# Performance work log

Hardware: AMD Instinct MI355X
Metric: run time of the kernel (lower is better)

The kernel has to match this reference:

```python
import jax, jax.numpy as jnp
import numpy as np

HIDDEN = 2048
N_EXPERTS = 8
TOP_K = 2
MOE_INTER = 1408
NORM_TOPK = False  # config.norm_topk_prob


def setup_inputs() -> dict:
    key = jax.random.key(0)
    k0, k1, k2, k3, k4 = jax.random.split(key, 5)
    hidden_states = jax.random.normal(k0, (2, 2048, HIDDEN), dtype=jnp.float32)
    # router gate: nn.Linear(hidden, num_experts, bias=False) -> store as [H, E]
    gate_w = jax.random.normal(k1, (HIDDEN, N_EXPERTS), dtype=jnp.float32) * 0.02
    # per-expert MLP weights, stacked over experts (Linear is x @ W.T, stored pre-transposed)
    w_gate = jax.random.normal(k2, (N_EXPERTS, HIDDEN, MOE_INTER), dtype=jnp.float32) * 0.02
    w_up = jax.random.normal(k3, (N_EXPERTS, HIDDEN, MOE_INTER), dtype=jnp.float32) * 0.02
    w_down = jax.random.normal(k4, (N_EXPERTS, MOE_INTER, HIDDEN), dtype=jnp.float32) * 0.02
    return {"hidden_states": hidden_states, "gate_w": gate_w,
            "w_gate": w_gate, "w_up": w_up, "w_down": w_down}


def reference(hidden_states, gate_w, w_gate, w_up, w_down):
    B, S, H = hidden_states.shape
    x = hidden_states.reshape(-1, H)                      # [T, H]
    T = x.shape[0]
    router_logits = x @ gate_w                            # [T, E]
    probs = jax.nn.softmax(router_logits.astype(jnp.float32), axis=-1)
    routing_weights, selected = jax.lax.top_k(probs, TOP_K)  # [T, K], [T, K]
    if NORM_TOPK:
        routing_weights = routing_weights / routing_weights.sum(-1, keepdims=True)
    routing_weights = routing_weights.astype(x.dtype)
    # dense combine weights [T, E]: scatter top-k weights to expert slots
    combine = jnp.zeros((T, N_EXPERTS), dtype=x.dtype)
    combine = combine.at[jnp.arange(T)[:, None], selected].add(routing_weights)
    # run all experts densely (reference form of gather-MLP-scatter)
    g = jnp.einsum('th,ehf->tef', x, w_gate)              # [T, E, F]
    u = jnp.einsum('th,ehf->tef', x, w_up)
    h = jax.nn.silu(g) * u
    y = jnp.einsum('tef,efh->teh', h, w_down)             # [T, E, H]
    out = jnp.einsum('te,teh->th', combine, y)            # [T, H]
    return out
```

## Files before the change

### kernel.cpp

```cpp
#include <hip/hip_runtime.h>
#include <hip/hip_bf16.h>

#define HID  2048
#define NEXP 8
#define FINT 1408
#define TM   256
#define BK   32
#define GU_NPAN 88
#define DN_NPAN 64

typedef __bf16 bf16_t;
typedef __bf16 bf16x8 __attribute__((ext_vector_type(8)));
typedef float  f32x4  __attribute__((ext_vector_type(4)));

#define AS1 __attribute__((address_space(1)))
#define AS3 __attribute__((address_space(3)))

__device__ __forceinline__ void gll16(const void* g, void* l) {
    __builtin_amdgcn_global_load_lds((const AS1 void*)g, (AS3 void*)l, 16, 0, 0);
}

#define VMCNT4() asm volatile("s_waitcnt vmcnt(4)" ::: "memory")
#define VMCNT0() asm volatile("s_waitcnt vmcnt(0)" ::: "memory")
#define SB0() __builtin_amdgcn_sched_barrier(0)

__global__ __launch_bounds__(64) void router_kernel(
    const float* __restrict__ x, const float* __restrict__ gw,
    int* __restrict__ cnt, int* __restrict__ topk_id, float* __restrict__ topk_w,
    bf16_t* __restrict__ xb, int T)
{
    int t = blockIdx.x;
    if (t >= T) return;
    int lane = threadIdx.x;
    float acc[NEXP];
#pragma unroll
    for (int e = 0; e < NEXP; ++e) acc[e] = 0.f;
    const float* xr = x + (size_t)t * HID;
    bf16_t* xo = xb + (size_t)t * HID;
    for (int i = lane; i < HID; i += 64) {
        float xv = xr[i];
        xo[i] = (bf16_t)xv;
        const float4* g4 = (const float4*)(gw + (size_t)i * NEXP);
        float4 a = g4[0], b = g4[1];
        acc[0] += xv * a.x; acc[1] += xv * a.y; acc[2] += xv * a.z; acc[3] += xv * a.w;
        acc[4] += xv * b.x; acc[5] += xv * b.y; acc[6] += xv * b.z; acc[7] += xv * b.w;
    }
#pragma unroll
    for (int d = 1; d < 64; d <<= 1) {
#pragma unroll
        for (int e = 0; e < NEXP; ++e) acc[e] += __shfl_xor(acc[e], d, 64);
    }
    float mx = acc[0];
#pragma unroll
    for (int e = 1; e < NEXP; ++e) mx = fmaxf(mx, acc[e]);
    float p[NEXP]; float s = 0.f;
#pragma unroll
    for (int e = 0; e < NEXP; ++e) { p[e] = expf(acc[e] - mx); s += p[e]; }
    float inv = 1.f / s;
    int i1 = 0;
#pragma unroll
    for (int e = 1; e < NEXP; ++e) if (acc[e] > acc[i1]) i1 = e;
    int i2 = (i1 == 0) ? 1 : 0;
#pragma unroll
    for (int e = 0; e < NEXP; ++e) if (e != i1 && acc[e] > acc[i2]) i2 = e;
    if (lane == 0) {
        topk_id[t * 2 + 0] = i1; topk_id[t * 2 + 1] = i2;
        topk_w[t * 2 + 0] = p[i1] * inv; topk_w[t * 2 + 1] = p[i2] * inv;
        atomicAdd(&cnt[i1], 1); atomicAdd(&cnt[i2], 1);
    }
}

__global__ void offsets_kernel(const int* __restrict__ cnt, int* __restrict__ offs,
                               int* __restrict__ gbase, int* __restrict__ gcount,
                               int* __restrict__ dbase, int* __restrict__ dcount,
                               int* __restrict__ gu, int* __restrict__ dn)
{
    if (threadIdx.x == 0) {
        int s = 0;
        for (int e = 0; e < NEXP; ++e) { offs[e] = s; s += cnt[e]; }
        offs[NEXP] = s;
        int k = 0;
        for (int x = 0; x < 8; ++x) {
            gbase[x] = k;
            for (int p = x; p < GU_NPAN; p += 8) {
                int e = p / 11, fp = p - e * 11;
                int nt = (cnt[e] + TM - 1) / TM;
                for (int t = 0; t < nt; ++t) gu[k++] = (e << 10) | (fp << 6) | t;
            }
            gcount[x] = k - gbase[x];
        }
        k = 0;
        for (int x = 0; x < 8; ++x) {
            dbase[x] = k;
            for (int p = x; p < DN_NPAN; p += 8) {
                int e = p >> 3, hp = p & 7;
                int nt = (cnt[e] + TM - 1) / TM;
                for (int t = 0; t < nt; ++t) dn[k++] = (e << 10) | (hp << 6) | t;
            }
            dcount[x] = k - dbase[x];
        }
    }
}

__global__ void scatter_kernel(
    const int* __restrict__ topk_id, const int* __restrict__ offs, int* __restrict__ fill,
    int* __restrict__ tok, int* __restrict__ slot_of, int T)
{
    int t = blockIdx.x * blockDim.x + threadIdx.x;
    if (t >= T) return;
#pragma unroll
    for (int k = 0; k < 2; ++k) {
        int e = topk_id[t * 2 + k];
        int pos = atomicAdd(&fill[e], 1);
        int slot = offs[e] + pos;
        tok[slot] = t;
        slot_of[t * 2 + k] = slot;
    }
}

__global__ __launch_bounds__(256) void cvt_t_kernel(
    const float* __restrict__ in, bf16_t* __restrict__ outb, int R, int C)
{
    int tilesR = R >> 6, tilesC = C >> 6;
    int per = tilesR * tilesC;
    int e = blockIdx.x / per;
    int rem = blockIdx.x - e * per;
    int tr = rem / tilesC, tc = rem - tr * tilesC;
    const float* src = in + (size_t)e * R * C + (size_t)(tr * 64) * C + tc * 64;
    bf16_t* dst = outb + (size_t)e * R * C + (size_t)(tc * 64) * R + tr * 64;

    __shared__ float tile[64][65];
    int tid = threadIdx.x;
    int rr = tid >> 4;
    int cc = (tid & 15) * 4;
#pragma unroll
    for (int i = 0; i < 4; ++i) {
        float4 v = *(const float4*)(src + (size_t)(rr + i * 16) * C + cc);
        tile[rr + i * 16][cc + 0] = v.x; tile[rr + i * 16][cc + 1] = v.y;
        tile[rr + i * 16][cc + 2] = v.z; tile[rr + i * 16][cc + 3] = v.w;
    }
    __syncthreads();
    int oc = tid >> 2;
    int og = (tid & 3) * 16;
    bf16_t* dp = dst + (size_t)oc * R + og;
    bf16x8 o0, o1;
#pragma unroll
    for (int j = 0; j < 8; ++j) { o0[j] = (bf16_t)tile[og + j][oc]; o1[j] = (bf16_t)tile[og + 8 + j][oc]; }
    *(bf16x8*)dp = o0;
    *(bf16x8*)(dp + 8) = o1;
}

__global__ __launch_bounds__(512, 2) void gateup3_kernel(
    const bf16_t* __restrict__ xb, const bf16_t* __restrict__ wgb, const bf16_t* __restrict__ wub,
    const int* __restrict__ offs, const int* __restrict__ tok,
    const int* __restrict__ gbase, const int* __restrict__ gcount, const int* __restrict__ gu,
    bf16_t* __restrict__ h_buf)
{
    __shared__ bf16_t smem[49152];
    const int tid = threadIdx.x;
    const int lane = tid & 63, w = tid >> 6;
    const int wm = w >> 1, wn = w & 1;
    const int lr = lane & 15, lg = lane >> 4;
    const int rl = lane >> 2;
    const int sw8 = ((lane & 3) ^ ((lane >> 3) & 3)) * 8;
    const int ksw = (lg ^ ((lr >> 1) & 3)) * 8;

    const int xcd = blockIdx.x & 7, slot = blockIdx.x >> 3;
    const int icnt = gcount[xcd], ib = gbase[xcd];

    for (int ii = slot; ii < icnt; ii += 32) {
        const int it = gu[ib + ii];
        const int e = it >> 10, fp = (it >> 6) & 15, tr = it & 63;
        const int seg0 = offs[e];
        const int rbase = tr * TM;
        const int nvalid = min(offs[e + 1] - seg0 - rbase, TM);
        const int row0 = seg0 + rbase;
        const int f0 = fp * 128;

        const bf16_t* aP[2];
#pragma unroll
        for (int i = 0; i < 2; ++i) {
            int r = (w * 2 + i) * 16 + rl;
            int tk = tok[row0 + min(r, nvalid - 1)];
            aP[i] = xb + (size_t)tk * HID + sw8;
        }
        const bf16_t* bP[2];
#pragma unroll
        for (int i = 0; i < 2; ++i) {
            int br = (w * 2 + i) * 16 + rl;
            const bf16_t* W = (br < 128) ? wgb : wub;
            bP[i] = W + ((size_t)e * FINT + f0 + (br & 127)) * HID + sw8;
        }

        f32x4 acc[4][8];
#pragma unroll
        for (int mi = 0; mi < 4; ++mi)
#pragma unroll
            for (int ni = 0; ni < 8; ++ni) acc[mi][ni] = (f32x4){0.f, 0.f, 0.f, 0.f};

        auto STAGE = [&](int b, int kt) {
            int k0 = kt * BK;
            bf16_t* A = smem + b * 8192;
            bf16_t* B = smem + 24576 + b * 8192;
            gll16(aP[0] + k0, A + (w * 2 + 0) * 512);
            gll16(aP[1] + k0, A + (w * 2 + 1) * 512);
            gll16(bP[0] + k0, B + (w * 2 + 0) * 512);
            gll16(bP[1] + k0, B + (w * 2 + 1) * 512);
        };
        auto COMPUTE = [&](int b) {
            const bf16_t* A = smem + b * 8192;
            const bf16_t* B = smem + 24576 + b * 8192;
            bf16x8 bfr[8];
#pragma unroll
            for (int ni = 0; ni < 8; ++ni)
                bfr[ni] = *(const bf16x8*)&B[(wn * 128 + ni * 16 + lr) * BK + ksw];
#pragma unroll
            for (int mi = 0; mi < 4; ++mi) {
                bf16x8 a = *(const bf16x8*)&A[(wm * 64 + mi * 16 + lr) * BK + ksw];
#pragma unroll
                for (int ni = 0; ni < 8; ++ni)
                    acc[mi][ni] = __builtin_amdgcn_mfma_f32_16x16x32_bf16(a, bfr[ni], acc[mi][ni], 0, 0, 0);
            }
        };

        const int NK = HID / BK;
        STAGE(0, 0); STAGE(1, 1);
        int c0 = 0, c1 = 1, c2 = 2;
        for (int kt = 0; kt < NK; ++kt) {
            SB0();
            if (kt + 1 < NK) { VMCNT4(); } else { VMCNT0(); }
            __builtin_amdgcn_s_barrier();
            SB0();
            if (kt + 2 < NK) STAGE(c2, kt + 2);
            SB0();
            COMPUTE(c0);
            int t = c0; c0 = c1; c1 = c2; c2 = t;
        }
        __syncthreads();

        if (wn == 1) {
#pragma unroll
            for (int mi = 0; mi < 4; ++mi)
#pragma unroll
                for (int ni = 0; ni < 8; ++ni)
#pragma unroll
                    for (int rr = 0; rr < 4; ++rr) {
                        int row = wm * 64 + mi * 16 + lg * 4 + rr;
                        int col = ni * 16 + lr;
                        smem[row * 128 + col] = (bf16_t)acc[mi][ni][rr];
                    }
        }
        __syncthreads();
        if (wn == 0) {
#pragma unroll
            for (int mi = 0; mi < 4; ++mi)
#pragma unroll
                for (int ni = 0; ni < 8; ++ni)
#pragma unroll
                    for (int rr = 0; rr < 4; ++rr) {
                        int row = wm * 64 + mi * 16 + lg * 4 + rr;
                        int col = ni * 16 + lr;
                        float g = acc[mi][ni][rr];
                        float u = (float)smem[row * 128 + col];
                        float h = (g / (1.f + __expf(-g))) * u;
                        if (row < nvalid)
                            h_buf[(size_t)(row0 + row) * FINT + f0 + col] = (bf16_t)h;
                    }
        }
        __syncthreads();
    }
}

__global__ __launch_bounds__(512, 2) void down3_kernel(
    const bf16_t* __restrict__ h_buf, const bf16_t* __restrict__ wdb,
    const int* __restrict__ offs,
    const int* __restrict__ dbase, const int* __restrict__ dcount, const int* __restrict__ dn,
    bf16_t* __restrict__ y_buf)
{
    __shared__ bf16_t smem[49152];
    const int tid = threadIdx.x;
    const int lane = tid & 63, w = tid >> 6;
    const int wm = w >> 1, wn = w & 1;
    const int lr = lane & 15, lg = lane >> 4;
    const int rl = lane >> 2;
    const int sw8 = ((lane & 3) ^ ((lane >> 3) & 3)) * 8;
    const int ksw = (lg ^ ((lr >> 1) & 3)) * 8;

    const int xcd = blockIdx.x & 7, slot = blockIdx.x >> 3;
    const int icnt = dcount[xcd], ib = dbase[xcd];

    for (int ii = slot; ii < icnt; ii += 32) {
        const int it = dn[ib + ii];
        const int e = it >> 10, hp = (it >> 6) & 15, tr = it & 63;
        const int seg0 = offs[e];
        const int rbase = tr * TM;
        const int nvalid = min(offs[e + 1] - seg0 - rbase, TM);
        const int row0 = seg0 + rbase;
        const int h0 = hp * 256;

        const bf16_t* aP[2];
#pragma unroll
        for (int i = 0; i < 2; ++i) {
            int r = (w * 2 + i) * 16 + rl;
            aP[i] = h_buf + (size_t)(row0 + r) * FINT + sw8;
        }
        const bf16_t* bP[2];
#pragma unroll
        for (int i = 0; i < 2; ++i) {
            int br = (w * 2 + i) * 16 + rl;
            bP[i] = wdb + ((size_t)e * HID + h0 + br) * FINT + sw8;
        }

        f32x4 acc[4][8];
#pragma unroll
        for (int mi = 0; mi < 4; ++mi)
#pragma unroll
            for (int ni = 0; ni < 8; ++ni) acc[mi][ni] = (f32x4){0.f, 0.f, 0.f, 0.f};

        auto STAGE = [&](int b, int kt) {
            int k0 = kt * BK;
            bf16_t* A = smem + b * 8192;
            bf16_t* B = smem + 24576 + b * 8192;
            gll16(aP[0] + k0, A + (w * 2 + 0) * 512);
            gll16(aP[1] + k0, A + (w * 2 + 1) * 512);
            gll16(bP[0] + k0, B + (w * 2 + 0) * 512);
            gll16(bP[1] + k0, B + (w * 2 + 1) * 512);
        };
        auto COMPUTE = [&](int b) {
            const bf16_t* A = smem + b * 8192;
            const bf16_t* B = smem + 24576 + b * 8192;
            bf16x8 bfr[8];
#pragma unroll
            for (int ni = 0; ni < 8; ++ni)
                bfr[ni] = *(const bf16x8*)&B[(wn * 128 + ni * 16 + lr) * BK + ksw];
#pragma unroll
            for (int mi = 0; mi < 4; ++mi) {
                bf16x8 a = *(const bf16x8*)&A[(wm * 64 + mi * 16 + lr) * BK + ksw];
#pragma unroll
                for (int ni = 0; ni < 8; ++ni)
                    acc[mi][ni] = __builtin_amdgcn_mfma_f32_16x16x32_bf16(a, bfr[ni], acc[mi][ni], 0, 0, 0);
            }
        };

        const int NK = FINT / BK;
        STAGE(0, 0); STAGE(1, 1);
        int c0 = 0, c1 = 1, c2 = 2;
        for (int kt = 0; kt < NK; ++kt) {
            SB0();
            if (kt + 1 < NK) { VMCNT4(); } else { VMCNT0(); }
            __builtin_amdgcn_s_barrier();
            SB0();
            if (kt + 2 < NK) STAGE(c2, kt + 2);
            SB0();
            COMPUTE(c0);
            int t = c0; c0 = c1; c1 = c2; c2 = t;
        }

#pragma unroll
        for (int mi = 0; mi < 4; ++mi)
#pragma unroll
            for (int ni = 0; ni < 8; ++ni)
#pragma unroll
                for (int rr = 0; rr < 4; ++rr) {
                    int row = wm * 64 + mi * 16 + lg * 4 + rr;
                    int col = wn * 128 + ni * 16 + lr;
                    if (row < nvalid)
                        y_buf[(size_t)(row0 + row) * HID + h0 + col] = (bf16_t)acc[mi][ni][rr];
                }
        __syncthreads();
    }
}

__global__ __launch_bounds__(256) void combine_kernel(
    const bf16_t* __restrict__ y, const int* __restrict__ slot_of,
    const float* __restrict__ topk_w, float* __restrict__ out, int T)
{
    int t = blockIdx.x;
    int tid = threadIdx.x;
    int s0 = slot_of[t * 2], s1 = slot_of[t * 2 + 1];
    float w0 = topk_w[t * 2], w1 = topk_w[t * 2 + 1];
    const bf16x8* y0 = (const bf16x8*)(y + (size_t)s0 * HID);
    const bf16x8* y1 = (const bf16x8*)(y + (size_t)s1 * HID);
    bf16x8 v0 = y0[tid], v1 = y1[tid];
    float* op = out + (size_t)t * HID + tid * 8;
#pragma unroll
    for (int j = 0; j < 8; ++j)
        op[j] = w0 * (float)v0[j] + w1 * (float)v1[j];
}

extern "C" void kernel_launch(void* const* d_in, const int* in_sizes, int n_in,
                              void* d_out, int out_size, void* d_ws, size_t ws_size,
                              hipStream_t stream)
{
    const float* x  = (const float*)d_in[0];
    const float* gw = (const float*)d_in[1];
    const float* wg = (const float*)d_in[2];
    const float* wu = (const float*)d_in[3];
    const float* wd = (const float*)d_in[4];
    float* out = (float*)d_out;
    int T = in_sizes[0] / HID;
    int S2 = 2 * T;

    char* base = (char*)d_ws;
    int* cnt     = (int*)base;
    int* fill    = cnt + 8;
    int* offs    = cnt + 16;
    int* gbase   = cnt + 32;
    int* gcount  = cnt + 40;
    int* dbase   = cnt + 48;
    int* dcount  = cnt + 56;
    int* gu      = cnt + 64;
    int* dnl     = cnt + 576;
    int* topk_id = cnt + 960;
    float* topk_w = (float*)(topk_id + S2);
    int* tok     = (int*)(topk_w + S2);
    int* slot_of = tok + S2 + 256;
    size_t small_end = (size_t)((char*)(slot_of + S2) - base);
    size_t cur = (small_end + 255) & ~(size_t)255;
    auto take = [&](size_t bytes) -> size_t {
        size_t o = cur; cur += bytes; cur = (cur + 255) & ~(size_t)255; return o;
    };
    size_t wbytes = (size_t)NEXP * HID * FINT * 2;
    size_t o_xb  = take((size_t)T * HID * 2);
    size_t o_wgb = take(wbytes);
    size_t o_wub = take(wbytes);
    size_t o_wdb = take(wbytes);
    size_t o_h   = take((size_t)(S2 + 256) * FINT * 2);
    size_t o_y   = take((size_t)(S2 + 256) * HID * 2);
    (void)ws_size;

    bf16_t* xb    = (bf16_t*)(base + o_xb);
    bf16_t* wgb   = (bf16_t*)(base + o_wgb);
    bf16_t* wub   = (bf16_t*)(base + o_wub);
    bf16_t* wdb   = (bf16_t*)(base + o_wdb);
    bf16_t* h_buf = (bf16_t*)(base + o_h);
    bf16_t* y_buf = (bf16_t*)(base + o_y);

    hipMemsetAsync(base, 0, 64, stream);

    router_kernel<<<T, 64, 0, stream>>>(x, gw, cnt, topk_id, topk_w, xb, T);
    offsets_kernel<<<1, 64, 0, stream>>>(cnt, offs, gbase, gcount, dbase, dcount, gu, dnl);
    scatter_kernel<<<(T + 255) / 256, 256, 0, stream>>>(topk_id, offs, fill, tok, slot_of, T);

    int gridW = NEXP * (HID / 64) * (FINT / 64);
    cvt_t_kernel<<<gridW, 256, 0, stream>>>(wg, wgb, HID, FINT);
    cvt_t_kernel<<<gridW, 256, 0, stream>>>(wu, wub, HID, FINT);
    cvt_t_kernel<<<gridW, 256, 0, stream>>>(wd, wdb, FINT, HID);

    gateup3_kernel<<<256, 512, 0, stream>>>(xb, wgb, wub, offs, tok, gbase, gcount, gu, h_buf);
    down3_kernel<<<256, 512, 0, stream>>>(h_buf, wdb, offs, dbase, dcount, dnl, y_buf);
    combine_kernel<<<T, 256, 0, stream>>>(y_buf, slot_of, topk_w, out, T);
}
```

Before: 493.4 us.

## Interleave split B staging with MFMA halves, fuse weight converts, parallelize offsets

The GEMM main loops in both expert kernels now split the B-tile global-to-LDS staging into two halves. Each half is interleaved with one half of the MFMA work, using explicit lgkmcnt waits and s_setprio to raise wave priority during the MFMA blocks. This also cuts live B fragment registers from 8 to 4. The three weight convert-transpose launches are merged into one kernel, and the offsets kernel builds its schedule lists with 16 threads instead of one, reducing launch and serial overhead. The lgkmcnt(0) waits could serialize LDS reads with the MFMAs.

```diff
diff --git a/kernel.cpp b/kernel.cpp
--- a/kernel.cpp
+++ b/kernel.cpp
@@ -22,6 +22,7 @@
 
 #define VMCNT4() asm volatile("s_waitcnt vmcnt(4)" ::: "memory")
 #define VMCNT0() asm volatile("s_waitcnt vmcnt(0)" ::: "memory")
+#define LGKM0()  asm volatile("s_waitcnt lgkmcnt(0)" ::: "memory")
 #define SB0() __builtin_amdgcn_sched_barrier(0)
 
 __global__ __launch_bounds__(64) void router_kernel(
@@ -75,29 +76,43 @@
                                int* __restrict__ dbase, int* __restrict__ dcount,
                                int* __restrict__ gu, int* __restrict__ dn)
 {
-    if (threadIdx.x == 0) {
+    __shared__ int gc[8], dc[8];
+    int tid = threadIdx.x;
+    if (tid == 0) {
         int s = 0;
         for (int e = 0; e < NEXP; ++e) { offs[e] = s; s += cnt[e]; }
         offs[NEXP] = s;
-        int k = 0;
-        for (int x = 0; x < 8; ++x) {
-            gbase[x] = k;
-            for (int p = x; p < GU_NPAN; p += 8) {
-                int e = p / 11, fp = p - e * 11;
-                int nt = (cnt[e] + TM - 1) / TM;
-                for (int t = 0; t < nt; ++t) gu[k++] = (e << 10) | (fp << 6) | t;
-            }
-            gcount[x] = k - gbase[x];
-        }
-        k = 0;
-        for (int x = 0; x < 8; ++x) {
-            dbase[x] = k;
-            for (int p = x; p < DN_NPAN; p += 8) {
-                int e = p >> 3, hp = p & 7;
-                int nt = (cnt[e] + TM - 1) / TM;
-                for (int t = 0; t < nt; ++t) dn[k++] = (e << 10) | (hp << 6) | t;
-            }
-            dcount[x] = k - dbase[x];
+    }
+    if (tid < 8) {
+        int c = 0;
+        for (int p = tid; p < GU_NPAN; p += 8) { int e = p / 11; c += (cnt[e] + TM - 1) / TM; }
+        gc[tid] = c;
+    } else if (tid < 16) {
+        int x = tid - 8, c = 0;
+        for (int p = x; p < DN_NPAN; p += 8) { int e = p >> 3; c += (cnt[e] + TM - 1) / TM; }
+        dc[x] = c;
+    }
+    __syncthreads();
+    if (tid < 8) {
+        int base = 0;
+        for (int i = 0; i < tid; ++i) base += gc[i];
+        gbase[tid] = base; gcount[tid] = gc[tid];
+        int k = base;
+        for (int p = tid; p < GU_NPAN; p += 8) {
+            int e = p / 11, fp = p - e * 11;
+            int nt = (cnt[e] + TM - 1) / TM;
+            for (int t = 0; t < nt; ++t) gu[k++] = (e << 10) | (fp << 6) | t;
+        }
+    } else if (tid < 16) {
+        int x = tid - 8;
+        int base = 0;
+        for (int i = 0; i < x; ++i) base += dc[i];
+        dbase[x] = base; dcount[x] = dc[x];
+        int k = base;
+        for (int p = x; p < DN_NPAN; p += 8) {
+            int e = p >> 3, hp = p & 7;
+            int nt = (cnt[e] + TM - 1) / TM;
+            for (int t = 0; t < nt; ++t) dn[k++] = (e << 10) | (hp << 6) | t;
         }
     }
 }
@@ -118,13 +133,21 @@
     }
 }
 
-__global__ __launch_bounds__(256) void cvt_t_kernel(
-    const float* __restrict__ in, bf16_t* __restrict__ outb, int R, int C)
-{
-    int tilesR = R >> 6, tilesC = C >> 6;
-    int per = tilesR * tilesC;
-    int e = blockIdx.x / per;
-    int rem = blockIdx.x - e * per;
+__global__ __launch_bounds__(256) void cvt3_kernel(
+    const float* __restrict__ wg, const float* __restrict__ wu, const float* __restrict__ wd,
+    bf16_t* __restrict__ wgb, bf16_t* __restrict__ wub, bf16_t* __restrict__ wdb)
+{
+    const int per = NEXP * (HID / 64) * (FINT / 64);
+    int b = blockIdx.x;
+    const float* in; bf16_t* outb; int R, C;
+    if (b < per)            { in = wg; outb = wgb; R = HID;  C = FINT; }
+    else if (b < 2 * per)   { b -= per; in = wu; outb = wub; R = HID;  C = FINT; }
+    else                    { b -= 2 * per; in = wd; outb = wdb; R = FINT; C = HID; }
+
+    int tilesC = C >> 6;
+    int perE = (R >> 6) * tilesC;
+    int e = b / perE;
+    int rem = b - e * perE;
     int tr = rem / tilesC, tc = rem - tr * tilesC;
     const float* src = in + (size_t)e * R * C + (size_t)(tr * 64) * C + tc * 64;
     bf16_t* dst = outb + (size_t)e * R * C + (size_t)(tc * 64) * R + tr * 64;
@@ -198,42 +221,59 @@
 #pragma unroll
             for (int ni = 0; ni < 8; ++ni) acc[mi][ni] = (f32x4){0.f, 0.f, 0.f, 0.f};
 
-        auto STAGE = [&](int b, int kt) {
+        auto STAGE_A = [&](int b, int kt) {
             int k0 = kt * BK;
             bf16_t* A = smem + b * 8192;
-            bf16_t* B = smem + 24576 + b * 8192;
             gll16(aP[0] + k0, A + (w * 2 + 0) * 512);
             gll16(aP[1] + k0, A + (w * 2 + 1) * 512);
+        };
+        auto STAGE_B = [&](int b, int kt) {
+            int k0 = kt * BK;
+            bf16_t* B = smem + 24576 + b * 8192;
             gll16(bP[0] + k0, B + (w * 2 + 0) * 512);
             gll16(bP[1] + k0, B + (w * 2 + 1) * 512);
         };
-        auto COMPUTE = [&](int b) {
-            const bf16_t* A = smem + b * 8192;
-            const bf16_t* B = smem + 24576 + b * 8192;
-            bf16x8 bfr[8];
-#pragma unroll
-            for (int ni = 0; ni < 8; ++ni)
-                bfr[ni] = *(const bf16x8*)&B[(wn * 128 + ni * 16 + lr) * BK + ksw];
-#pragma unroll
-            for (int mi = 0; mi < 4; ++mi) {
-                bf16x8 a = *(const bf16x8*)&A[(wm * 64 + mi * 16 + lr) * BK + ksw];
-#pragma unroll
-                for (int ni = 0; ni < 8; ++ni)
-                    acc[mi][ni] = __builtin_amdgcn_mfma_f32_16x16x32_bf16(a, bfr[ni], acc[mi][ni], 0, 0, 0);
-            }
-        };
 
         const int NK = HID / BK;
-        STAGE(0, 0); STAGE(1, 1);
+        STAGE_A(0, 0); STAGE_B(0, 0); STAGE_A(1, 1); STAGE_B(1, 1);
         int c0 = 0, c1 = 1, c2 = 2;
         for (int kt = 0; kt < NK; ++kt) {
             SB0();
             if (kt + 1 < NK) { VMCNT4(); } else { VMCNT0(); }
             __builtin_amdgcn_s_barrier();
             SB0();
-            if (kt + 2 < NK) STAGE(c2, kt + 2);
-            SB0();
-            COMPUTE(c0);
+            const bf16_t* A = smem + c0 * 8192;
+            const bf16_t* B = smem + 24576 + c0 * 8192;
+            if (kt + 2 < NK) STAGE_A(c2, kt + 2);
+            bf16x8 afr[4], bfr[4];
+#pragma unroll
+            for (int mi = 0; mi < 4; ++mi)
+                afr[mi] = *(const bf16x8*)&A[(wm * 64 + mi * 16 + lr) * BK + ksw];
+#pragma unroll
+            for (int ni = 0; ni < 4; ++ni)
+                bfr[ni] = *(const bf16x8*)&B[(wn * 128 + ni * 16 + lr) * BK + ksw];
+            LGKM0(); SB0();
+            __builtin_amdgcn_s_setprio(1);
+#pragma unroll
+            for (int mi = 0; mi < 4; ++mi)
+#pragma unroll
+                for (int ni = 0; ni < 4; ++ni)
+                    acc[mi][ni] = __builtin_amdgcn_mfma_f32_16x16x32_bf16(afr[mi], bfr[ni], acc[mi][ni], 0, 0, 0);
+            __builtin_amdgcn_s_setprio(0);
+            SB0();
+            if (kt + 2 < NK) STAGE_B(c2, kt + 2);
+#pragma unroll
+            for (int ni = 0; ni < 4; ++ni)
+                bfr[ni] = *(const bf16x8*)&B[(wn * 128 + (ni + 4) * 16 + lr) * BK + ksw];
+            LGKM0(); SB0();
+            __builtin_amdgcn_s_setprio(1);
+#pragma unroll
+            for (int mi = 0; mi < 4; ++mi)
+#pragma unroll
+                for (int ni = 0; ni < 4; ++ni)
+                    acc[mi][ni + 4] = __builtin_amdgcn_mfma_f32_16x16x32_bf16(afr[mi], bfr[ni], acc[mi][ni + 4], 0, 0, 0);
+            __builtin_amdgcn_s_setprio(0);
+            SB0();
             int t = c0; c0 = c1; c1 = c2; c2 = t;
         }
         __syncthreads();
@@ -317,42 +357,59 @@
 #pragma unroll
             for (int ni = 0; ni < 8; ++ni) acc[mi][ni] = (f32x4){0.f, 0.f, 0.f, 0.f};
 
-        auto STAGE = [&](int b, int kt) {
+        auto STAGE_A = [&](int b, int kt) {
             int k0 = kt * BK;
             bf16_t* A = smem + b * 8192;
-            bf16_t* B = smem + 24576 + b * 8192;
             gll16(aP[0] + k0, A + (w * 2 + 0) * 512);
             gll16(aP[1] + k0, A + (w * 2 + 1) * 512);
+        };
+        auto STAGE_B = [&](int b, int kt) {
+            int k0 = kt * BK;
+            bf16_t* B = smem + 24576 + b * 8192;
             gll16(bP[0] + k0, B + (w * 2 + 0) * 512);
             gll16(bP[1] + k0, B + (w * 2 + 1) * 512);
         };
-        auto COMPUTE = [&](int b) {
-            const bf16_t* A = smem + b * 8192;
-            const bf16_t* B = smem + 24576 + b * 8192;
-            bf16x8 bfr[8];
-#pragma unroll
-            for (int ni = 0; ni < 8; ++ni)
-                bfr[ni] = *(const bf16x8*)&B[(wn * 128 + ni * 16 + lr) * BK + ksw];
-#pragma unroll
-            for (int mi = 0; mi < 4; ++mi) {
-                bf16x8 a = *(const bf16x8*)&A[(wm * 64 + mi * 16 + lr) * BK + ksw];
-#pragma unroll
-                for (int ni = 0; ni < 8; ++ni)
-                    acc[mi][ni] = __builtin_amdgcn_mfma_f32_16x16x32_bf16(a, bfr[ni], acc[mi][ni], 0, 0, 0);
-            }
-        };
 
         const int NK = FINT / BK;
-        STAGE(0, 0); STAGE(1, 1);
+        STAGE_A(0, 0); STAGE_B(0, 0); STAGE_A(1, 1); STAGE_B(1, 1);
         int c0 = 0, c1 = 1, c2 = 2;
         for (int kt = 0; kt < NK; ++kt) {
             SB0();
             if (kt + 1 < NK) { VMCNT4(); } else { VMCNT0(); }
             __builtin_amdgcn_s_barrier();
             SB0();
-            if (kt + 2 < NK) STAGE(c2, kt + 2);
-            SB0();
-            COMPUTE(c0);
+            const bf16_t* A = smem + c0 * 8192;
+            const bf16_t* B = smem + 24576 + c0 * 8192;
+            if (kt + 2 < NK) STAGE_A(c2, kt + 2);
+            bf16x8 afr[4], bfr[4];
+#pragma unroll
+            for (int mi = 0; mi < 4; ++mi)
+                afr[mi] = *(const bf16x8*)&A[(wm * 64 + mi * 16 + lr) * BK + ksw];
+#pragma unroll
+            for (int ni = 0; ni < 4; ++ni)
+                bfr[ni] = *(const bf16x8*)&B[(wn * 128 + ni * 16 + lr) * BK + ksw];
+            LGKM0(); SB0();
+            __builtin_amdgcn_s_setprio(1);
+#pragma unroll
+            for (int mi = 0; mi < 4; ++mi)
+#pragma unroll
+                for (int ni = 0; ni < 4; ++ni)
+                    acc[mi][ni] = __builtin_amdgcn_mfma_f32_16x16x32_bf16(afr[mi], bfr[ni], acc[mi][ni], 0, 0, 0);
+            __builtin_amdgcn_s_setprio(0);
+            SB0();
+            if (kt + 2 < NK) STAGE_B(c2, kt + 2);
+#pragma unroll
+            for (int ni = 0; ni < 4; ++ni)
+                bfr[ni] = *(const bf16x8*)&B[(wn * 128 + (ni + 4) * 16 + lr) * BK + ksw];
+            LGKM0(); SB0();
+            __builtin_amdgcn_s_setprio(1);
+#pragma unroll
+            for (int mi = 0; mi < 4; ++mi)
+#pragma unroll
+                for (int ni = 0; ni < 4; ++ni)
+                    acc[mi][ni + 4] = __builtin_amdgcn_mfma_f32_16x16x32_bf16(afr[mi], bfr[ni], acc[mi][ni + 4], 0, 0, 0);
+            __builtin_amdgcn_s_setprio(0);
+            SB0();
             int t = c0; c0 = c1; c1 = c2; c2 = t;
         }
 
@@ -442,10 +499,8 @@
     offsets_kernel<<<1, 64, 0, stream>>>(cnt, offs, gbase, gcount, dbase, dcount, gu, dnl);
     scatter_kernel<<<(T + 255) / 256, 256, 0, stream>>>(topk_id, offs, fill, tok, slot_of, T);
 
-    int gridW = NEXP * (HID / 64) * (FINT / 64);
-    cvt_t_kernel<<<gridW, 256, 0, stream>>>(wg, wgb, HID, FINT);
-    cvt_t_kernel<<<gridW, 256, 0, stream>>>(wu, wub, HID, FINT);
-    cvt_t_kernel<<<gridW, 256, 0, stream>>>(wd, wdb, FINT, HID);
+    int gridW = 3 * NEXP * (HID / 64) * (FINT / 64);
+    cvt3_kernel<<<gridW, 256, 0, stream>>>(wg, wu, wd, wgb, wub, wdb);
 
     gateup3_kernel<<<256, 512, 0, stream>>>(xb, wgb, wub, offs, tok, gbase, gcount, gu, h_buf);
     down3_kernel<<<256, 512, 0, stream>>>(h_buf, wdb, offs, dbase, dcount, dnl, y_buf);
```

Result: faster. 469.4 us (-4.9%).

## Fuse router and weight conversion, double-buffer GEMMs for higher occupancy

Applied to the files above, without the earlier changes.

The router and the three weight transpose/convert launches are merged into one prep kernel, and the router now handles four tokens per block with vectorized loads. Both grouped GEMMs drop from triple to double buffering, which cuts LDS use so four blocks fit per CU, and they launch with twice the grid. The offsets kernel is parallelized across 16 threads. The cost is an extra barrier per k-step and a shallower prefetch pipeline, which may expose more load latency.

```diff
diff --git a/kernel.cpp b/kernel.cpp
--- a/kernel.cpp
+++ b/kernel.cpp
@@ -23,51 +23,100 @@
 #define VMCNT4() asm volatile("s_waitcnt vmcnt(4)" ::: "memory")
 #define VMCNT0() asm volatile("s_waitcnt vmcnt(0)" ::: "memory")
 #define SB0() __builtin_amdgcn_sched_barrier(0)
-
-__global__ __launch_bounds__(64) void router_kernel(
+#define BAR() __builtin_amdgcn_s_barrier()
+
+__global__ __launch_bounds__(256) void prep_kernel(
     const float* __restrict__ x, const float* __restrict__ gw,
     int* __restrict__ cnt, int* __restrict__ topk_id, float* __restrict__ topk_w,
-    bf16_t* __restrict__ xb, int T)
-{
-    int t = blockIdx.x;
-    if (t >= T) return;
-    int lane = threadIdx.x;
-    float acc[NEXP];
-#pragma unroll
-    for (int e = 0; e < NEXP; ++e) acc[e] = 0.f;
-    const float* xr = x + (size_t)t * HID;
-    bf16_t* xo = xb + (size_t)t * HID;
-    for (int i = lane; i < HID; i += 64) {
-        float xv = xr[i];
-        xo[i] = (bf16_t)xv;
-        const float4* g4 = (const float4*)(gw + (size_t)i * NEXP);
-        float4 a = g4[0], b = g4[1];
-        acc[0] += xv * a.x; acc[1] += xv * a.y; acc[2] += xv * a.z; acc[3] += xv * a.w;
-        acc[4] += xv * b.x; acc[5] += xv * b.y; acc[6] += xv * b.z; acc[7] += xv * b.w;
-    }
-#pragma unroll
-    for (int d = 1; d < 64; d <<= 1) {
-#pragma unroll
-        for (int e = 0; e < NEXP; ++e) acc[e] += __shfl_xor(acc[e], d, 64);
-    }
-    float mx = acc[0];
-#pragma unroll
-    for (int e = 1; e < NEXP; ++e) mx = fmaxf(mx, acc[e]);
-    float p[NEXP]; float s = 0.f;
-#pragma unroll
-    for (int e = 0; e < NEXP; ++e) { p[e] = expf(acc[e] - mx); s += p[e]; }
-    float inv = 1.f / s;
-    int i1 = 0;
-#pragma unroll
-    for (int e = 1; e < NEXP; ++e) if (acc[e] > acc[i1]) i1 = e;
-    int i2 = (i1 == 0) ? 1 : 0;
-#pragma unroll
-    for (int e = 0; e < NEXP; ++e) if (e != i1 && acc[e] > acc[i2]) i2 = e;
-    if (lane == 0) {
-        topk_id[t * 2 + 0] = i1; topk_id[t * 2 + 1] = i2;
-        topk_w[t * 2 + 0] = p[i1] * inv; topk_w[t * 2 + 1] = p[i2] * inv;
-        atomicAdd(&cnt[i1], 1); atomicAdd(&cnt[i2], 1);
-    }
+    bf16_t* __restrict__ xb, int T,
+    const float* __restrict__ wg, const float* __restrict__ wu, const float* __restrict__ wd,
+    bf16_t* __restrict__ wgb, bf16_t* __restrict__ wub, bf16_t* __restrict__ wdb)
+{
+    const int RB = T / 4;
+    const int per = NEXP * (HID / 64) * (FINT / 64);
+    __shared__ float tile[64][65];
+
+    if ((int)blockIdx.x < RB) {
+        int tid = threadIdx.x;
+        int lane = tid & 63, w = tid >> 6;
+        int t = blockIdx.x * 4 + w;
+        if (t >= T) return;
+        float acc[NEXP];
+#pragma unroll
+        for (int e = 0; e < NEXP; ++e) acc[e] = 0.f;
+        const float* xr = x + (size_t)t * HID;
+        bf16_t* xo = xb + (size_t)t * HID;
+        for (int i0 = lane * 4; i0 < HID; i0 += 256) {
+            float4 xv = *(const float4*)(xr + i0);
+            bf16_t b4[4] = {(bf16_t)xv.x, (bf16_t)xv.y, (bf16_t)xv.z, (bf16_t)xv.w};
+            *(uint2*)(xo + i0) = *(uint2*)b4;
+            float xs[4] = {xv.x, xv.y, xv.z, xv.w};
+#pragma unroll
+            for (int u = 0; u < 4; ++u) {
+                const float4* g4 = (const float4*)(gw + (size_t)(i0 + u) * NEXP);
+                float4 a = g4[0], b = g4[1];
+                acc[0] += xs[u] * a.x; acc[1] += xs[u] * a.y; acc[2] += xs[u] * a.z; acc[3] += xs[u] * a.w;
+                acc[4] += xs[u] * b.x; acc[5] += xs[u] * b.y; acc[6] += xs[u] * b.z; acc[7] += xs[u] * b.w;
+            }
+        }
+#pragma unroll
+        for (int d = 1; d < 64; d <<= 1) {
+#pragma unroll
+            for (int e = 0; e < NEXP; ++e) acc[e] += __shfl_xor(acc[e], d, 64);
+        }
+        float mx = acc[0];
+#pragma unroll
+        for (int e = 1; e < NEXP; ++e) mx = fmaxf(mx, acc[e]);
+        float p[NEXP]; float s = 0.f;
+#pragma unroll
+        for (int e = 0; e < NEXP; ++e) { p[e] = expf(acc[e] - mx); s += p[e]; }
+        float inv = 1.f / s;
+        int i1 = 0;
+#pragma unroll
+        for (int e = 1; e < NEXP; ++e) if (acc[e] > acc[i1]) i1 = e;
+        int i2 = (i1 == 0) ? 1 : 0;
+#pragma unroll
+        for (int e = 0; e < NEXP; ++e) if (e != i1 && acc[e] > acc[i2]) i2 = e;
+        if (lane == 0) {
+            topk_id[t * 2 + 0] = i1; topk_id[t * 2 + 1] = i2;
+            topk_w[t * 2 + 0] = p[i1] * inv; topk_w[t * 2 + 1] = p[i2] * inv;
+            atomicAdd(&cnt[i1], 1); atomicAdd(&cnt[i2], 1);
+        }
+        return;
+    }
+
+    int b = blockIdx.x - RB;
+    const float* in; bf16_t* outb; int R, C;
+    if (b < per)            { in = wg; outb = wgb; R = HID;  C = FINT; }
+    else if (b < 2 * per)   { b -= per; in = wu; outb = wub; R = HID;  C = FINT; }
+    else                    { b -= 2 * per; in = wd; outb = wdb; R = FINT; C = HID; }
+
+    int tilesC = C >> 6;
+    int perE = (R >> 6) * tilesC;
+    int e = b / perE;
+    int rem = b - e * perE;
+    int tr = rem / tilesC, tc = rem - tr * tilesC;
+    const float* src = in + (size_t)e * R * C + (size_t)(tr * 64) * C + tc * 64;
+    bf16_t* dst = outb + (size_t)e * R * C + (size_t)(tc * 64) * R + tr * 64;
+
+    int tid = threadIdx.x;
+    int rr = tid >> 4;
+    int cc = (tid & 15) * 4;
+#pragma unroll
+    for (int i = 0; i < 4; ++i) {
+        float4 v = *(const float4*)(src + (size_t)(rr + i * 16) * C + cc);
+        tile[rr + i * 16][cc + 0] = v.x; tile[rr + i * 16][cc + 1] = v.y;
+        tile[rr + i * 16][cc + 2] = v.z; tile[rr + i * 16][cc + 3] = v.w;
+    }
+    __syncthreads();
+    int oc = tid >> 2;
+    int og = (tid & 3) * 16;
+    bf16_t* dp = dst + (size_t)oc * R + og;
+    bf16x8 o0, o1;
+#pragma unroll
+    for (int j = 0; j < 8; ++j) { o0[j] = (bf16_t)tile[og + j][oc]; o1[j] = (bf16_t)tile[og + 8 + j][oc]; }
+    *(bf16x8*)dp = o0;
+    *(bf16x8*)(dp + 8) = o1;
 }
 
 __global__ void offsets_kernel(const int* __restrict__ cnt, int* __restrict__ offs,
@@ -75,29 +124,43 @@
                                int* __restrict__ dbase, int* __restrict__ dcount,
                                int* __restrict__ gu, int* __restrict__ dn)
 {
-    if (threadIdx.x == 0) {
+    __shared__ int gc[8], dc[8];
+    int tid = threadIdx.x;
+    if (tid == 0) {
         int s = 0;
         for (int e = 0; e < NEXP; ++e) { offs[e] = s; s += cnt[e]; }
         offs[NEXP] = s;
-        int k = 0;
-        for (int x = 0; x < 8; ++x) {
-            gbase[x] = k;
-            for (int p = x; p < GU_NPAN; p += 8) {
-                int e = p / 11, fp = p - e * 11;
-                int nt = (cnt[e] + TM - 1) / TM;
-                for (int t = 0; t < nt; ++t) gu[k++] = (e << 10) | (fp << 6) | t;
-            }
-            gcount[x] = k - gbase[x];
-        }
-        k = 0;
-        for (int x = 0; x < 8; ++x) {
-            dbase[x] = k;
-            for (int p = x; p < DN_NPAN; p += 8) {
-                int e = p >> 3, hp = p & 7;
-                int nt = (cnt[e] + TM - 1) / TM;
-                for (int t = 0; t < nt; ++t) dn[k++] = (e << 10) | (hp << 6) | t;
-            }
-            dcount[x] = k - dbase[x];
+    }
+    if (tid < 8) {
+        int c = 0;
+        for (int p = tid; p < GU_NPAN; p += 8) { int e = p / 11; c += (cnt[e] + TM - 1) / TM; }
+        gc[tid] = c;
+    } else if (tid < 16) {
+        int x = tid - 8, c = 0;
+        for (int p = x; p < DN_NPAN; p += 8) { int e = p >> 3; c += (cnt[e] + TM - 1) / TM; }
+        dc[x] = c;
+    }
+    __syncthreads();
+    if (tid < 8) {
+        int base = 0;
+        for (int i = 0; i < tid; ++i) base += gc[i];
+        gbase[tid] = base; gcount[tid] = gc[tid];
+        int k = base;
+        for (int p = tid; p < GU_NPAN; p += 8) {
+            int e = p / 11, fp = p - e * 11;
+            int nt = (cnt[e] + TM - 1) / TM;
+            for (int t = 0; t < nt; ++t) gu[k++] = (e << 10) | (fp << 6) | t;
+        }
+    } else if (tid < 16) {
+        int x = tid - 8;
+        int base = 0;
+        for (int i = 0; i < x; ++i) base += dc[i];
+        dbase[x] = base; dcount[x] = dc[x];
+        int k = base;
+        for (int p = x; p < DN_NPAN; p += 8) {
+            int e = p >> 3, hp = p & 7;
+            int nt = (cnt[e] + TM - 1) / TM;
+            for (int t = 0; t < nt; ++t) dn[k++] = (e << 10) | (hp << 6) | t;
         }
     }
 }
@@ -118,45 +181,13 @@
     }
 }
 
-__global__ __launch_bounds__(256) void cvt_t_kernel(
-    const float* __restrict__ in, bf16_t* __restrict__ outb, int R, int C)
-{
-    int tilesR = R >> 6, tilesC = C >> 6;
-    int per = tilesR * tilesC;
-    int e = blockIdx.x / per;
-    int rem = blockIdx.x - e * per;
-    int tr = rem / tilesC, tc = rem - tr * tilesC;
-    const float* src = in + (size_t)e * R * C + (size_t)(tr * 64) * C + tc * 64;
-    bf16_t* dst = outb + (size_t)e * R * C + (size_t)(tc * 64) * R + tr * 64;
-
-    __shared__ float tile[64][65];
-    int tid = threadIdx.x;
-    int rr = tid >> 4;
-    int cc = (tid & 15) * 4;
-#pragma unroll
-    for (int i = 0; i < 4; ++i) {
-        float4 v = *(const float4*)(src + (size_t)(rr + i * 16) * C + cc);
-        tile[rr + i * 16][cc + 0] = v.x; tile[rr + i * 16][cc + 1] = v.y;
-        tile[rr + i * 16][cc + 2] = v.z; tile[rr + i * 16][cc + 3] = v.w;
-    }
-    __syncthreads();
-    int oc = tid >> 2;
-    int og = (tid & 3) * 16;
-    bf16_t* dp = dst + (size_t)oc * R + og;
-    bf16x8 o0, o1;
-#pragma unroll
-    for (int j = 0; j < 8; ++j) { o0[j] = (bf16_t)tile[og + j][oc]; o1[j] = (bf16_t)tile[og + 8 + j][oc]; }
-    *(bf16x8*)dp = o0;
-    *(bf16x8*)(dp + 8) = o1;
-}
-
-__global__ __launch_bounds__(512, 2) void gateup3_kernel(
+__global__ __launch_bounds__(512, 4) void gateup6_kernel(
     const bf16_t* __restrict__ xb, const bf16_t* __restrict__ wgb, const bf16_t* __restrict__ wub,
     const int* __restrict__ offs, const int* __restrict__ tok,
     const int* __restrict__ gbase, const int* __restrict__ gcount, const int* __restrict__ gu,
     bf16_t* __restrict__ h_buf)
 {
-    __shared__ bf16_t smem[49152];
+    __shared__ bf16_t smem[32768];
     const int tid = threadIdx.x;
     const int lane = tid & 63, w = tid >> 6;
     const int wm = w >> 1, wn = w & 1;
@@ -168,7 +199,7 @@
     const int xcd = blockIdx.x & 7, slot = blockIdx.x >> 3;
     const int icnt = gcount[xcd], ib = gbase[xcd];
 
-    for (int ii = slot; ii < icnt; ii += 32) {
+    for (int ii = slot; ii < icnt; ii += 64) {
         const int it = gu[ib + ii];
         const int e = it >> 10, fp = (it >> 6) & 15, tr = it & 63;
         const int seg0 = offs[e];
@@ -201,7 +232,7 @@
         auto STAGE = [&](int b, int kt) {
             int k0 = kt * BK;
             bf16_t* A = smem + b * 8192;
-            bf16_t* B = smem + 24576 + b * 8192;
+            bf16_t* B = smem + 16384 + b * 8192;
             gll16(aP[0] + k0, A + (w * 2 + 0) * 512);
             gll16(aP[1] + k0, A + (w * 2 + 1) * 512);
             gll16(bP[0] + k0, B + (w * 2 + 0) * 512);
@@ -209,7 +240,7 @@
         };
         auto COMPUTE = [&](int b) {
             const bf16_t* A = smem + b * 8192;
-            const bf16_t* B = smem + 24576 + b * 8192;
+            const bf16_t* B = smem + 16384 + b * 8192;
             bf16x8 bfr[8];
 #pragma unroll
             for (int ni = 0; ni < 8; ++ni)
@@ -224,17 +255,19 @@
         };
 
         const int NK = HID / BK;
-        STAGE(0, 0); STAGE(1, 1);
-        int c0 = 0, c1 = 1, c2 = 2;
+        STAGE(0, 0);
+        int cur = 0;
         for (int kt = 0; kt < NK; ++kt) {
-            SB0();
-            if (kt + 1 < NK) { VMCNT4(); } else { VMCNT0(); }
-            __builtin_amdgcn_s_barrier();
-            SB0();
-            if (kt + 2 < NK) STAGE(c2, kt + 2);
-            SB0();
-            COMPUTE(c0);
-            int t = c0; c0 = c1; c1 = c2; c2 = t;
+            const bool nl = (kt + 1 < NK);
+            if (nl) STAGE(cur ^ 1, kt + 1);
+            SB0();
+            if (nl) { VMCNT4(); } else { VMCNT0(); }
+            BAR();
+            SB0();
+            COMPUTE(cur);
+            SB0();
+            BAR();
+            cur ^= 1;
         }
         __syncthreads();
 
@@ -271,13 +304,13 @@
     }
 }
 
-__global__ __launch_bounds__(512, 2) void down3_kernel(
+__global__ __launch_bounds__(512, 4) void down6_kernel(
     const bf16_t* __restrict__ h_buf, const bf16_t* __restrict__ wdb,
     const int* __restrict__ offs,
     const int* __restrict__ dbase, const int* __restrict__ dcount, const int* __restrict__ dn,
     bf16_t* __restrict__ y_buf)
 {
-    __shared__ bf16_t smem[49152];
+    __shared__ bf16_t smem[32768];
     const int tid = threadIdx.x;
     const int lane = tid & 63, w = tid >> 6;
     const int wm = w >> 1, wn = w & 1;
@@ -289,7 +322,7 @@
     const int xcd = blockIdx.x & 7, slot = blockIdx.x >> 3;
     const int icnt = dcount[xcd], ib = dbase[xcd];
 
-    for (int ii = slot; ii < icnt; ii += 32) {
+    for (int ii = slot; ii < icnt; ii += 64) {
         const int it = dn[ib + ii];
         const int e = it >> 10, hp = (it >> 6) & 15, tr = it & 63;
         const int seg0 = offs[e];
@@ -320,7 +353,7 @@
         auto STAGE = [&](int b, int kt) {
             int k0 = kt * BK;
             bf16_t* A = smem + b * 8192;
-            bf16_t* B = smem + 24576 + b * 8192;
+            bf16_t* B = smem + 16384 + b * 8192;
             gll16(aP[0] + k0, A + (w * 2 + 0) * 512);
             gll16(aP[1] + k0, A + (w * 2 + 1) * 512);
             gll16(bP[0] + k0, B + (w * 2 + 0) * 512);
@@ -328,7 +361,7 @@
         };
         auto COMPUTE = [&](int b) {
             const bf16_t* A = smem + b * 8192;
-            const bf16_t* B = smem + 24576 + b * 8192;
+            const bf16_t* B = smem + 16384 + b * 8192;
             bf16x8 bfr[8];
 #pragma unroll
             for (int ni = 0; ni < 8; ++ni)
@@ -343,17 +376,19 @@
         };
 
         const int NK = FINT / BK;
-        STAGE(0, 0); STAGE(1, 1);
-        int c0 = 0, c1 = 1, c2 = 2;
+        STAGE(0, 0);
+        int cur = 0;
         for (int kt = 0; kt < NK; ++kt) {
-            SB0();
-            if (kt + 1 < NK) { VMCNT4(); } else { VMCNT0(); }
-            __builtin_amdgcn_s_barrier();
-            SB0();
-            if (kt + 2 < NK) STAGE(c2, kt + 2);
-            SB0();
-            COMPUTE(c0);
-            int t = c0; c0 = c1; c1 = c2; c2 = t;
+            const bool nl = (kt + 1 < NK);
+            if (nl) STAGE(cur ^ 1, kt + 1);
+            SB0();
+            if (nl) { VMCNT4(); } else { VMCNT0(); }
+            BAR();
+            SB0();
+            COMPUTE(cur);
+            SB0();
+            BAR();
+            cur ^= 1;
         }
 
 #pragma unroll
@@ -438,16 +473,14 @@
 
     hipMemsetAsync(base, 0, 64, stream);
 
-    router_kernel<<<T, 64, 0, stream>>>(x, gw, cnt, topk_id, topk_w, xb, T);
+    int RB = T / 4;
+    int gridPrep = RB + 3 * NEXP * (HID / 64) * (FINT / 64);
+    prep_kernel<<<gridPrep, 256, 0, stream>>>(x, gw, cnt, topk_id, topk_w, xb, T,
+                                              wg, wu, wd, wgb, wub, wdb);
     offsets_kernel<<<1, 64, 0, stream>>>(cnt, offs, gbase, gcount, dbase, dcount, gu, dnl);
     scatter_kernel<<<(T + 255) / 256, 256, 0, stream>>>(topk_id, offs, fill, tok, slot_of, T);
 
-    int gridW = NEXP * (HID / 64) * (FINT / 64);
-    cvt_t_kernel<<<gridW, 256, 0, stream>>>(wg, wgb, HID, FINT);
-    cvt_t_kernel<<<gridW, 256, 0, stream>>>(wu, wub, HID, FINT);
-    cvt_t_kernel<<<gridW, 256, 0, stream>>>(wd, wdb, FINT, HID);
-
-    gateup3_kernel<<<256, 512, 0, stream>>>(xb, wgb, wub, offs, tok, gbase, gcount, gu, h_buf);
-    down3_kernel<<<256, 512, 0, stream>>>(h_buf, wdb, offs, dbase, dcount, dnl, y_buf);
+    gateup6_kernel<<<512, 512, 0, stream>>>(xb, wgb, wub, offs, tok, gbase, gcount, gu, h_buf);
+    down6_kernel<<<512, 512, 0, stream>>>(h_buf, wdb, offs, dbase, dcount, dnl, y_buf);
     combine_kernel<<<T, 256, 0, stream>>>(y_buf, slot_of, topk_w, out, T);
 }
```

After: 1.826 ms. 3.7x slower.
